# Optimization experiments

Measured on AMD Instinct MI355X. Metric: run time of the kernel, lower is better.

## Reference

```python
import jax, jax.numpy as jnp
import numpy as np


def setup_inputs() -> dict:
    key = jax.random.key(0)
    T, DIM, NF = 500000, 64, 10000      # total atoms, feature dim, fingerprint vocab
    L_HID, L_OUT = 3, 2                 # layer_hidden, layer_output
    M, E = 20000, 2000000               # molecules, directed edges
    S = T // M                          # atoms per molecule (uniform blocks)
    ks = jax.random.split(key, 8)
    fingerprints = jax.random.randint(ks[0], (T,), 0, NF)
    # block-diagonal adjacency as edge list: neighbors stay inside the molecule block
    src = jax.random.randint(ks[1], (E,), 0, T)
    off = jax.random.randint(ks[2], (E,), 0, S)
    dst = (src // S) * S + off
    node_mol = jnp.repeat(jnp.arange(M), S)  # sorted segment ids, node -> molecule
    emb_table = jax.random.normal(ks[3], (NF, DIM), dtype=jnp.float32)
    W_fp = jax.random.normal(ks[4], (L_HID, DIM, DIM), dtype=jnp.float32) * 0.1
    b_fp = jnp.zeros((L_HID, DIM), dtype=jnp.float32)
    W_out = jax.random.normal(ks[5], (L_OUT, DIM, DIM), dtype=jnp.float32) * 0.1
    b_out = jnp.zeros((L_OUT, DIM), dtype=jnp.float32)
    W_prop = jax.random.normal(ks[6], (1, DIM), dtype=jnp.float32) * 0.1
    b_prop = jnp.zeros((1,), dtype=jnp.float32)
    return {"emb_table": emb_table, "W_fp": W_fp, "b_fp": b_fp,
            "W_out": W_out, "b_out": b_out, "W_prop": W_prop, "b_prop": b_prop,
            "fingerprints": fingerprints, "edge_src": src, "edge_dst": dst,
            "node_mol": node_mol, "num_mols": M}


def _l2_normalize(x):
    # F.normalize(x, p=2, dim=1): x / max(||x||_2, eps)
    n = jnp.sqrt(jnp.sum(x * x, axis=1, keepdims=True))
    return x / jnp.maximum(n, 1e-12)


def reference(emb_table, W_fp, b_fp, W_out, b_out, W_prop, b_prop,
              fingerprints, edge_src, edge_dst, node_mol, num_mols):
    # Embedding lookup: [T, dim]
    v = emb_table[fingerprints]
    # GNN layers: h = relu(Wv+b); v = normalize(h + A h)  (A = block-diag 0/1)
    for l in range(W_fp.shape[0]):
        h = jax.nn.relu(v @ W_fp[l].T + b_fp[l])
        agg = jnp.zeros_like(h).at[edge_dst].add(h[edge_src])  # (A h) via scatter-add
        v = _l2_normalize(h + agg)
    # Molecular vectors: sum of atom vectors per molecule -> [M, dim]
    mol = jax.ops.segment_sum(v, node_mol, num_segments=num_mols)
    # Output MLP
    for l in range(W_out.shape[0]):
        mol = jax.nn.relu(mol @ W_out[l].T + b_out[l])
    return mol @ W_prop.T + b_prop
```

## Files before the change

kernel.cpp:

```cpp
#include <hip/hip_runtime.h>
#include <hip/hip_bf16.h>
#include <stdint.h>

#define S_ATOMS 25
#define DIM 64
#define AP 40
#define VP 72
#define WAVES 4
#define PM 4
#define BMOLS 16
#define XB2 2560
#define EPB 8192
#define CAP 2048

typedef __attribute__((ext_vector_type(8))) short short8;
typedef __attribute__((ext_vector_type(4))) short short4s;
typedef __attribute__((ext_vector_type(4))) float f32x4;
typedef __attribute__((ext_vector_type(4))) unsigned uint4v;

static __device__ __forceinline__ short bf(float x) {
    return (short)__builtin_bit_cast(unsigned short, __float2bfloat16(x));
}
static __device__ __forceinline__ unsigned cvtpk(float lo, float hi) {
    unsigned r;
    asm("v_cvt_pk_bf16_f32 %0, %1, %2" : "=v"(r) : "v"(lo), "v"(hi));
    return r;
}

__global__ __launch_bounds__(256) void prep_k(
    const float* __restrict__ W_fp, const float* __restrict__ emb,
    unsigned* __restrict__ zbuf, short* __restrict__ wpk, short* __restrict__ embT,
    int LH, int NF, int nzero, int doEmb)
{
    int gid = blockIdx.x * 256 + threadIdx.x;
    if (gid < nzero) {
        uint4v z; z[0]=0; z[1]=0; z[2]=0; z[3]=0;
        ((uint4v*)zbuf)[gid] = z;
    }
    if (gid < LH * 512) {
        int t = gid;
        int layer = t >> 9, q = t & 511;
        int nt = q >> 7, ks = (q >> 6) & 1, lane = q & 63;
        int cc = lane & 15, gg = lane >> 4;
        const float* p = W_fp + (size_t)layer * 4096 + (nt * 16 + cc) * 64 + ks * 32 + 8 * gg;
        short8 s;
        #pragma unroll
        for (int j = 0; j < 8; ++j) s[j] = bf(p[j]);
        *(short8*)(wpk + (size_t)t * 8) = s;
    }
    if (doEmb && gid < NF * 8) {
        int row = gid >> 3, seg = gid & 7;
        const float* p = emb + (size_t)row * DIM + seg * 8;
        short8 s;
        #pragma unroll
        for (int j = 0; j < 8; ++j) s[j] = bf(p[j]);
        *(short8*)(embT + (size_t)row * DIM + seg * 8) = s;
    }
}

__global__ __launch_bounds__(256) void scatter_k(
    const int* __restrict__ esrc, const int* __restrict__ edst,
    unsigned* __restrict__ gcur, unsigned short* __restrict__ sorted,
    int E, int NBUK)
{
    extern __shared__ unsigned cnt[];
    for (int j = threadIdx.x; j < NBUK; j += 256) cnt[j] = 0;
    __syncthreads();
    int base = blockIdx.x * EPB;
    int end = base + EPB; if (end > E) end = E;
    int e = base + threadIdx.x * 4;
    for (; e + 4 <= end; e += 1024) {
        int4 s4 = *(const int4*)(esrc + e);
        atomicAdd(&cnt[(s4.x / S_ATOMS) >> 4], 1u);
        atomicAdd(&cnt[(s4.y / S_ATOMS) >> 4], 1u);
        atomicAdd(&cnt[(s4.z / S_ATOMS) >> 4], 1u);
        atomicAdd(&cnt[(s4.w / S_ATOMS) >> 4], 1u);
    }
    for (; e < end; ++e)
        atomicAdd(&cnt[(esrc[e] / S_ATOMS) >> 4], 1u);
    __syncthreads();
    for (int j = threadIdx.x; j < NBUK; j += 256) {
        unsigned cj = cnt[j];
        unsigned b0 = cj ? atomicAdd(&gcur[j], cj) : 0u;
        if (b0 > CAP) b0 = CAP;
        cnt[j] = (unsigned)j * CAP + b0;
    }
    __syncthreads();
    for (int e2 = base + threadIdx.x; e2 < end; e2 += 256) {
        int s = esrc[e2], d = edst[e2];
        int m  = s / S_ATOMS;
        int sl = s - m * S_ATOMS;
        int dl = d - m * S_ATOMS;
        int b  = m >> 4;
        unsigned pos = atomicAdd(&cnt[b], 1u);
        if (pos < (unsigned)(b + 1) * CAP)
            sorted[pos] = (unsigned short)((m & 15) * 640 + dl * 25 + sl);
    }
}

template<bool SORTED, bool FAST>
__global__ __launch_bounds__(256, 4) void gnn_k(
    const float* __restrict__ emb,
    const short* __restrict__ embT,
    const float* __restrict__ b_fp, const float* __restrict__ W_out,
    const float* __restrict__ b_out, const float* __restrict__ W_prop,
    const float* __restrict__ b_prop, const int* __restrict__ fps,
    const unsigned* __restrict__ Bg,
    const unsigned short* __restrict__ sorted,
    const unsigned* __restrict__ gcur,
    const short* __restrict__ wpk, float* __restrict__ out,
    int LH, int LO, int M)
{
    __shared__ __align__(16) short xb_all[WAVES][XB2];
    __shared__ __align__(16) float mv_all[WAVES][PM][DIM];
    __shared__ unsigned bh[BMOLS * 80];
    const int w = threadIdx.x >> 6, l = threadIdx.x & 63;
    const int c = l & 15, g = l >> 4;
    short* xb = xb_all[w];
    const short8* wp8 = (const short8*)wpk;
    const int wave_id = blockIdx.x * WAVES + w;

    if (SORTED) {
        for (int j = threadIdx.x; j < BMOLS * 80; j += 256) bh[j] = 0;
        __syncthreads();
        unsigned cb = gcur[blockIdx.x]; if (cb > CAP) cb = CAP;
        const unsigned short* sp = sorted + (size_t)blockIdx.x * CAP;
        for (int i = threadIdx.x; i < (int)cb; i += 256) {
            unsigned k = sp[i];
            atomicAdd(&bh[k >> 3], 1u << ((k & 7) * 4));
        }
        __syncthreads();
    }

    for (int mi = 0; mi < PM; ++mi) {
        const int mol = wave_id * PM + mi;
        if (mol >= M) break;

        const int ml = w * PM + mi;
        short8 amat[2];
        #pragma unroll
        for (int at = 0; at < 2; ++at) {
            int row = at * 16 + c;
            float f[8];
            if (row < S_ATOMS) {
                unsigned lo, hi; int sh;
                if (SORTED) {
                    int n0 = ml * 640 + row * 25 + 8 * g;
                    lo = bh[n0 >> 3]; hi = bh[(n0 >> 3) + 1];
                    sh = (n0 & 7) * 4;
                } else {
                    int n0 = mol * 625 + row * 25 + 8 * g;
                    lo = Bg[n0 >> 3]; hi = Bg[(n0 >> 3) + 1];
                    sh = (n0 & 7) * 4;
                }
                unsigned long long v64 = ((unsigned long long)hi << 32) | lo;
                v64 >>= sh;
                #pragma unroll
                for (int j = 0; j < 8; ++j) {
                    unsigned n = (unsigned)(v64 >> (4 * j)) & 0xFu;
                    f[j] = (8 * g + j) < S_ATOMS ? (float)n : 0.f;
                    if (8 * g + j == row) f[j] += 1.0f;
                }
            } else {
                #pragma unroll
                for (int j = 0; j < 8; ++j) f[j] = 0.f;
            }
            short8 s;
            #pragma unroll
            for (int j = 0; j < 8; ++j) s[j] = bf(f[j]);
            amat[at] = s;
        }

        short8 a1[2][2];
        #pragma unroll
        for (int mt = 0; mt < 2; ++mt) {
            int atom = mt * 16 + c;
            int aa = atom < S_ATOMS ? atom : S_ATOMS - 1;
            int fi = fps[mol * S_ATOMS + aa];
            #pragma unroll
            for (int ks = 0; ks < 2; ++ks) {
                if (FAST) {
                    a1[mt][ks] = *(const short8*)(embT + (size_t)fi * DIM + ks * 32 + 8 * g);
                } else {
                    const float4* qp = (const float4*)(emb + (size_t)fi * DIM + ks * 32 + 8 * g);
                    float4 f0 = qp[0], f1 = qp[1];
                    short8 s;
                    s[0]=bf(f0.x); s[1]=bf(f0.y); s[2]=bf(f0.z); s[3]=bf(f0.w);
                    s[4]=bf(f1.x); s[5]=bf(f1.y); s[6]=bf(f1.z); s[7]=bf(f1.w);
                    a1[mt][ks] = s;
                }
            }
        }

        for (int layer = 0; layer < LH; ++layer) {
            float bv[4];
            #pragma unroll
            for (int nt = 0; nt < 4; ++nt) bv[nt] = b_fp[layer * DIM + nt * 16 + c];
            f32x4 acc[2][4];
            #pragma unroll
            for (int mt = 0; mt < 2; ++mt)
                #pragma unroll
                for (int nt = 0; nt < 4; ++nt) {
                    f32x4 a; a[0]=bv[nt]; a[1]=bv[nt]; a[2]=bv[nt]; a[3]=bv[nt];
                    acc[mt][nt] = a;
                }
            #pragma unroll
            for (int ks = 0; ks < 2; ++ks) {
                short8 bwk[4];
                #pragma unroll
                for (int nt = 0; nt < 4; ++nt)
                    bwk[nt] = wp8[layer * 512 + nt * 128 + ks * 64 + l];
                #pragma unroll
                for (int mt = 0; mt < 2; ++mt)
                    #pragma unroll
                    for (int nt = 0; nt < 4; ++nt)
                        acc[mt][nt] = __builtin_amdgcn_mfma_f32_16x16x32_bf16(
                            a1[mt][ks], bwk[nt], acc[mt][nt], 0, 0, 0);
            }

            #pragma unroll
            for (int mt = 0; mt < 2; ++mt)
                #pragma unroll
                for (int nt = 0; nt < 4; ++nt) {
                    unsigned w0 = cvtpk(fmaxf(acc[mt][nt][0], 0.f),
                                        fmaxf(acc[mt][nt][1], 0.f));
                    unsigned w1 = cvtpk(fmaxf(acc[mt][nt][2], 0.f),
                                        fmaxf(acc[mt][nt][3], 0.f));
                    *(uint2*)&xb[(nt * 16 + c) * AP + mt * 16 + 4 * g] = make_uint2(w0, w1);
                }
            __builtin_amdgcn_wave_barrier();

            short8 b2[4];
            #pragma unroll
            for (int dt = 0; dt < 4; ++dt)
                b2[dt] = *(const short8*)&xb[(dt * 16 + c) * AP + 8 * g];
            f32x4 ua[4][2];
            #pragma unroll
            for (int dt = 0; dt < 4; ++dt)
                #pragma unroll
                for (int at = 0; at < 2; ++at) {
                    f32x4 z; z[0]=0.f; z[1]=0.f; z[2]=0.f; z[3]=0.f;
                    ua[dt][at] = __builtin_amdgcn_mfma_f32_16x16x32_bf16(
                        b2[dt], amat[at], z, 0, 0, 0);
                }

            float ss0 = 0.f, ss1 = 0.f;
            #pragma unroll
            for (int dt = 0; dt < 4; ++dt)
                #pragma unroll
                for (int r = 0; r < 4; ++r) {
                    ss0 += ua[dt][0][r] * ua[dt][0][r];
                    ss1 += ua[dt][1][r] * ua[dt][1][r];
                }
            ss0 += __shfl_xor(ss0, 16); ss0 += __shfl_xor(ss0, 32);
            ss1 += __shfl_xor(ss1, 16); ss1 += __shfl_xor(ss1, 32);
            float rn0 = __builtin_amdgcn_rsqf(fmaxf(ss0, 1e-24f));
            float rn1 = __builtin_amdgcn_rsqf(fmaxf(ss1, 1e-24f));

            bool lastl = (layer == LH - 1);
            __builtin_amdgcn_wave_barrier();
            if (!lastl) {
                #pragma unroll
                for (int at = 0; at < 2; ++at) {
                    float r0 = at ? rn1 : rn0;
                    #pragma unroll
                    for (int dt = 0; dt < 4; ++dt) {
                        unsigned w0 = cvtpk(ua[dt][at][0] * r0, ua[dt][at][1] * r0);
                        unsigned w1 = cvtpk(ua[dt][at][2] * r0, ua[dt][at][3] * r0);
                        *(uint2*)&xb[(at * 16 + c) * VP + dt * 16 + 4 * g] = make_uint2(w0, w1);
                    }
                }
                __builtin_amdgcn_wave_barrier();
                #pragma unroll
                for (int mt = 0; mt < 2; ++mt)
                    #pragma unroll
                    for (int ks = 0; ks < 2; ++ks)
                        a1[mt][ks] = *(const short8*)&xb[(mt * 16 + c) * VP + ks * 32 + 8 * g];
            } else {
                float mx[16];
                #pragma unroll
                for (int dt = 0; dt < 4; ++dt)
                    #pragma unroll
                    for (int r = 0; r < 4; ++r)
                        mx[dt * 4 + r] = ua[dt][0][r] * rn0 + ua[dt][1][r] * rn1;
                #pragma unroll
                for (int k = 0; k < 8; ++k) {
                    float send = (c & 8) ? mx[k] : mx[k + 8];
                    float keep = (c & 8) ? mx[k + 8] : mx[k];
                    mx[k] = keep + __shfl_xor(send, 8);
                }
                #pragma unroll
                for (int k = 0; k < 4; ++k) {
                    float send = (c & 4) ? mx[k] : mx[k + 4];
                    float keep = (c & 4) ? mx[k + 4] : mx[k];
                    mx[k] = keep + __shfl_xor(send, 4);
                }
                #pragma unroll
                for (int k = 0; k < 2; ++k) {
                    float send = (c & 2) ? mx[k] : mx[k + 2];
                    float keep = (c & 2) ? mx[k + 2] : mx[k];
                    mx[k] = keep + __shfl_xor(send, 2);
                }
                {
                    float send = (c & 1) ? mx[0] : mx[1];
                    float keep = (c & 1) ? mx[1] : mx[0];
                    mx[0] = keep + __shfl_xor(send, 1);
                }
                int dim = (c >> 2) * 16 + 4 * g + (c & 3);
                mv_all[w][mi][dim] = mx[0];
                __builtin_amdgcn_wave_barrier();
            }
        }
    }

    float cur[PM];
    for (int layer = 0; layer < LO; ++layer) {
        const float4* wr = (const float4*)(W_out + ((size_t)layer * DIM + l) * DIM);
        float bb = b_out[layer * DIM + l];
        float av[PM];
        #pragma unroll
        for (int q = 0; q < PM; ++q) av[q] = bb;
        #pragma unroll
        for (int k = 0; k < 16; ++k) {
            float4 ww = wr[k];
            #pragma unroll
            for (int q = 0; q < PM; ++q) {
                float4 vv = ((const float4*)mv_all[w][q])[k];
                av[q] += vv.x * ww.x + vv.y * ww.y + vv.z * ww.z + vv.w * ww.w;
            }
        }
        __builtin_amdgcn_wave_barrier();
        #pragma unroll
        for (int q = 0; q < PM; ++q) { cur[q] = fmaxf(av[q], 0.f); mv_all[w][q][l] = cur[q]; }
        __builtin_amdgcn_wave_barrier();
    }
    float wpv = W_prop[l], bp = b_prop[0];
    #pragma unroll
    for (int q = 0; q < PM; ++q) {
        float p = cur[q] * wpv;
        p += __shfl_xor(p, 1);  p += __shfl_xor(p, 2);
        p += __shfl_xor(p, 4);  p += __shfl_xor(p, 8);
        p += __shfl_xor(p, 16); p += __shfl_xor(p, 32);
        int mol = wave_id * PM + q;
        if (l == 0 && mol < M) out[mol] = p + bp;
    }
}

__global__ __launch_bounds__(256) void ehist_k(
    const int* __restrict__ esrc, const int* __restrict__ edst,
    unsigned* __restrict__ Bg, int E)
{
    int e = blockIdx.x * 256 + threadIdx.x;
    if (e >= E) return;
    int s = esrc[e], d = edst[e];
    int m  = s / S_ATOMS;
    int sl = s - m * S_ATOMS;
    int dl = d - m * S_ATOMS;
    int n = m * 625 + dl * 25 + sl;
    atomicAdd(&Bg[n >> 3], 1u << ((n & 7) * 4));
}

extern "C" void kernel_launch(void* const* d_in, const int* in_sizes, int n_in,
                              void* d_out, int out_size, void* d_ws, size_t ws_size,
                              hipStream_t stream)
{
    const float* emb    = (const float*)d_in[0];
    const float* W_fp   = (const float*)d_in[1];
    const float* b_fp   = (const float*)d_in[2];
    const float* W_out  = (const float*)d_in[3];
    const float* b_out  = (const float*)d_in[4];
    const float* W_prop = (const float*)d_in[5];
    const float* b_prop = (const float*)d_in[6];
    const int*   fps    = (const int*)d_in[7];
    const int*   esrc   = (const int*)d_in[8];
    const int*   edst   = (const int*)d_in[9];

    const int T  = in_sizes[7];
    const int E  = in_sizes[8];
    const int NF = in_sizes[0] / DIM;
    const int LH = in_sizes[1] / (DIM * DIM);
    const int LO = in_sizes[3] / (DIM * DIM);
    const int M  = T / S_ATOMS;

    const int NBUK = (M + BMOLS - 1) / BMOLS;
    const int NBLK = (E + EPB - 1) / EPB;
    const int grid = (M + WAVES * PM - 1) / (WAVES * PM);

    auto al = [](size_t x) { return (x + 255) & ~(size_t)255; };
    size_t sortedB = al((size_t)NBUK * CAP * 2);
    size_t gcurB   = al((size_t)NBUK * 4 + 16);
    size_t embT_b  = al((size_t)NF * DIM * 2);
    size_t wpk_b   = al((size_t)LH * 512 * 16);
    size_t histB   = al(((size_t)M * 625 + 1) / 2 + 16);

    float* outp = (float*)d_out;

    if (ws_size >= sortedB + gcurB + embT_b + wpk_b) {
        unsigned short* sorted = (unsigned short*)d_ws;
        unsigned* gcur = (unsigned*)((char*)d_ws + sortedB);
        short*    embT = (short*)((char*)d_ws + sortedB + gcurB);
        short*    wpk  = (short*)((char*)d_ws + sortedB + gcurB + embT_b);

        int nzero = (int)(gcurB / 16);
        int workP = NF * 8;
        if (LH * 512 > workP) workP = LH * 512;
        if (nzero > workP) workP = nzero;
        prep_k<<<(workP + 255) / 256, 256, 0, stream>>>(
            W_fp, emb, gcur, wpk, embT, LH, NF, nzero, 1);
        scatter_k<<<NBLK, 256, NBUK * 4, stream>>>(esrc, edst, gcur, sorted, E, NBUK);
        gnn_k<true, true><<<grid, WAVES * 64, 0, stream>>>(
            emb, embT, b_fp, W_out, b_out, W_prop, b_prop, fps,
            nullptr, sorted, gcur, wpk, outp, LH, LO, M);
    } else {
        bool fast = ws_size >= histB + embT_b + wpk_b;
        unsigned* Bg = (unsigned*)d_ws;
        short* embT = fast ? (short*)((char*)d_ws + histB) : nullptr;
        short* wpk  = fast ? (short*)((char*)d_ws + histB + embT_b)
                           : (short*)((char*)d_ws + histB);
        int nzero = (int)(histB / 16);
        int workP = nzero;
        if (fast && NF * 8 > workP) workP = NF * 8;
        if (LH * 512 > workP) workP = LH * 512;
        prep_k<<<(workP + 255) / 256, 256, 0, stream>>>(
            W_fp, emb, Bg, wpk, embT, LH, NF, nzero, fast ? 1 : 0);
        ehist_k<<<(E + 255) / 256, 256, 0, stream>>>(esrc, edst, Bg, E);
        if (fast)
            gnn_k<false, true><<<grid, WAVES * 64, 0, stream>>>(
                emb, embT, b_fp, W_out, b_out, W_prop, b_prop, fps,
                Bg, nullptr, nullptr, wpk, outp, LH, LO, M);
        else
            gnn_k<false, false><<<grid, WAVES * 64, 0, stream>>>(
                emb, embT, b_fp, W_out, b_out, W_prop, b_prop, fps,
                Bg, nullptr, nullptr, wpk, outp, LH, LO, M);
    }
}
```

Measured before the change: 101.2 us.

## Fold bf16 weight and embedding conversion into scatter kernel, enlarge molecule buckets

The W_fp and embedding-table bf16 conversion moves from prep_k into scatter_k as grid-stride loops, leaving prep_k to only zero the bucket counters. This shrinks the serial prep launch and overlaps the conversion with edge bucketing. Each GNN workgroup now covers 20 molecules (5 per wave) instead of 16, with matching bucket sizing (CAP, EPB). That gives fewer, heavier blocks and bucket-sort blocks, at some cost to occupancy and shared-memory use.

```diff
diff --git a/kernel.cpp b/kernel.cpp
--- a/kernel.cpp
+++ b/kernel.cpp
@@ -7,11 +7,11 @@
 #define AP 40
 #define VP 72
 #define WAVES 4
-#define PM 4
-#define BMOLS 16
+#define PM 5
+#define BMOLS 20
 #define XB2 2560
-#define EPB 8192
-#define CAP 2048
+#define EPB 16384
+#define CAP 2560
 
 typedef __attribute__((ext_vector_type(8))) short short8;
 typedef __attribute__((ext_vector_type(4))) short short4s;
@@ -61,9 +61,32 @@
 __global__ __launch_bounds__(256) void scatter_k(
     const int* __restrict__ esrc, const int* __restrict__ edst,
     unsigned* __restrict__ gcur, unsigned short* __restrict__ sorted,
-    int E, int NBUK)
+    const float* __restrict__ W_fp, const float* __restrict__ emb,
+    short* __restrict__ wpk, short* __restrict__ embT,
+    int E, int NBUK, int LH, int NF)
 {
     extern __shared__ unsigned cnt[];
+    int gid = blockIdx.x * 256 + threadIdx.x;
+    int gs  = gridDim.x * 256;
+    for (int t = gid; t < LH * 512; t += gs) {
+        int layer = t >> 9, q = t & 511;
+        int nt = q >> 7, ks = (q >> 6) & 1, lane = q & 63;
+        int cc = lane & 15, gg = lane >> 4;
+        const float* p = W_fp + (size_t)layer * 4096 + (nt * 16 + cc) * 64 + ks * 32 + 8 * gg;
+        short8 s;
+        #pragma unroll
+        for (int j = 0; j < 8; ++j) s[j] = bf(p[j]);
+        *(short8*)(wpk + (size_t)t * 8) = s;
+    }
+    for (int t = gid; t < NF * 8; t += gs) {
+        int row = t >> 3, seg = t & 7;
+        const float* p = emb + (size_t)row * DIM + seg * 8;
+        short8 s;
+        #pragma unroll
+        for (int j = 0; j < 8; ++j) s[j] = bf(p[j]);
+        *(short8*)(embT + (size_t)row * DIM + seg * 8) = s;
+    }
+
     for (int j = threadIdx.x; j < NBUK; j += 256) cnt[j] = 0;
     __syncthreads();
     int base = blockIdx.x * EPB;
@@ -71,13 +94,13 @@
     int e = base + threadIdx.x * 4;
     for (; e + 4 <= end; e += 1024) {
         int4 s4 = *(const int4*)(esrc + e);
-        atomicAdd(&cnt[(s4.x / S_ATOMS) >> 4], 1u);
-        atomicAdd(&cnt[(s4.y / S_ATOMS) >> 4], 1u);
-        atomicAdd(&cnt[(s4.z / S_ATOMS) >> 4], 1u);
-        atomicAdd(&cnt[(s4.w / S_ATOMS) >> 4], 1u);
+        atomicAdd(&cnt[s4.x / (S_ATOMS * BMOLS)], 1u);
+        atomicAdd(&cnt[s4.y / (S_ATOMS * BMOLS)], 1u);
+        atomicAdd(&cnt[s4.z / (S_ATOMS * BMOLS)], 1u);
+        atomicAdd(&cnt[s4.w / (S_ATOMS * BMOLS)], 1u);
     }
     for (; e < end; ++e)
-        atomicAdd(&cnt[(esrc[e] / S_ATOMS) >> 4], 1u);
+        atomicAdd(&cnt[esrc[e] / (S_ATOMS * BMOLS)], 1u);
     __syncthreads();
     for (int j = threadIdx.x; j < NBUK; j += 256) {
         unsigned cj = cnt[j];
@@ -91,10 +114,11 @@
         int m  = s / S_ATOMS;
         int sl = s - m * S_ATOMS;
         int dl = d - m * S_ATOMS;
-        int b  = m >> 4;
+        int b  = s / (S_ATOMS * BMOLS);
+        int ml = m - b * BMOLS;
         unsigned pos = atomicAdd(&cnt[b], 1u);
         if (pos < (unsigned)(b + 1) * CAP)
-            sorted[pos] = (unsigned short)((m & 15) * 640 + dl * 25 + sl);
+            sorted[pos] = (unsigned short)(ml * 640 + dl * 25 + sl);
     }
 }
 
@@ -402,12 +426,10 @@
         short*    wpk  = (short*)((char*)d_ws + sortedB + gcurB + embT_b);
 
         int nzero = (int)(gcurB / 16);
-        int workP = NF * 8;
-        if (LH * 512 > workP) workP = LH * 512;
-        if (nzero > workP) workP = nzero;
-        prep_k<<<(workP + 255) / 256, 256, 0, stream>>>(
-            W_fp, emb, gcur, wpk, embT, LH, NF, nzero, 1);
-        scatter_k<<<NBLK, 256, NBUK * 4, stream>>>(esrc, edst, gcur, sorted, E, NBUK);
+        prep_k<<<(nzero + 255) / 256, 256, 0, stream>>>(
+            W_fp, emb, gcur, wpk, embT, 0, NF, nzero, 0);
+        scatter_k<<<NBLK, 256, NBUK * 4, stream>>>(
+            esrc, edst, gcur, sorted, W_fp, emb, wpk, embT, E, NBUK, LH, NF);
         gnn_k<true, true><<<grid, WAVES * 64, 0, stream>>>(
             emb, embT, b_fp, W_out, b_out, W_prop, b_prop, fps,
             nullptr, sorted, gcur, wpk, outp, LH, LO, M);
```

After: 111.8 us. 10.5% more time.
